# Performance work log

Hardware: AMD Instinct MI355X
Metric: run time of the kernel (lower is better)

## Reference

```python
import jax, jax.numpy as jnp
import numpy as np

CODEBOOK_SIZE = 32768
EMBED_DIM = 32
BETA = 0.25


def setup_inputs() -> dict:
    key = jax.random.key(0)
    k_z, k_cb = jax.random.split(key)
    z = jax.random.normal(k_z, (4, EMBED_DIM, 32, 32), dtype=jnp.float32)
    codebook = jax.random.normal(k_cb, (CODEBOOK_SIZE, EMBED_DIM), dtype=jnp.float32)
    return {"z": z, "codebook": codebook}


def reference(z, codebook):
    # z: [B, C, H, W] -> flatten to [N, C] tokens (channel-last, as in torch VQ)
    B, C, H, W = z.shape
    zf = jnp.transpose(z, (0, 2, 3, 1)).reshape(-1, C)  # [N, C]
    # squared L2 distance to every code: ||z||^2 - 2 z.e + ||e||^2  -> [N, K]
    d = (
        jnp.sum(zf * zf, axis=-1, keepdims=True)
        - 2.0 * (zf @ codebook.T)
        + jnp.sum(codebook * codebook, axis=-1)[None, :]
    )
    idx = jnp.argmin(d, axis=-1)  # [N]
    zq = codebook[idx].reshape(B, H, W, C).transpose(0, 3, 1, 2)  # [B, C, H, W]
    # codebook + commitment losses
    loss = jnp.mean((jax.lax.stop_gradient(zq) - z) ** 2) + BETA * jnp.mean(
        (zq - jax.lax.stop_gradient(z)) ** 2
    )
    # straight-through estimator
    zq_st = z + jax.lax.stop_gradient(zq - z)
    return zq_st, loss
```

## Files before the change

kernel.cpp:

```cpp
#include <hip/hip_runtime.h>
#include <math.h>

#define K_CB    32768
#define C_DIM   32
#define N_TOK   4096
#define OUT_N   (N_TOK * C_DIM)

#define SLICES  32
#define KPERSL  (K_CB / SLICES)
#define GROUPS  (KPERSL / 16)
#define SCALE   4096.0f

typedef _Float16 half8  __attribute__((ext_vector_type(8)));
typedef float    floatx4 __attribute__((ext_vector_type(4)));

__global__ __launch_bounds__(256) void vq_zprep(const float* __restrict__ z,
                                                _Float16* __restrict__ zh,
                                                _Float16* __restrict__ zl) {
    const int tok = blockIdx.x * 256 + threadIdx.x;
    const int b = tok >> 10, hw = tok & 1023;
    const float* zp = z + (size_t)b * (C_DIM * 1024) + hw;
    _Float16 h[C_DIM], l[C_DIM];
#pragma unroll
    for (int c = 0; c < C_DIM; ++c) {
        float xs = zp[(size_t)c * 1024] * SCALE;
        _Float16 hh = (_Float16)xs;
        h[c] = hh;
        l[c] = (_Float16)(xs - (float)hh);
    }
    half8* dh = (half8*)(zh + (size_t)tok * C_DIM);
    half8* dl = (half8*)(zl + (size_t)tok * C_DIM);
#pragma unroll
    for (int i = 0; i < 4; ++i) {
        dh[i] = *(half8*)&h[i * 8];
        dl[i] = *(half8*)&l[i * 8];
    }
}

__global__ __launch_bounds__(256) void vq_cbprep(const float* __restrict__ cb,
                                                 _Float16* __restrict__ ch,
                                                 _Float16* __restrict__ cl,
                                                 float* __restrict__ nrm,
                                                 float* __restrict__ out) {
    const int k = blockIdx.x * 256 + threadIdx.x;
    const float4* src = (const float4*)(cb + (size_t)k * C_DIM);
    _Float16 h[C_DIM], l[C_DIM];
    float s = 0.f;
#pragma unroll
    for (int i = 0; i < 8; ++i) {
        float4 v = src[i];
        s = fmaf(v.x, v.x, s); s = fmaf(v.y, v.y, s);
        s = fmaf(v.z, v.z, s); s = fmaf(v.w, v.w, s);
        float x[4] = {v.x * SCALE, v.y * SCALE, v.z * SCALE, v.w * SCALE};
#pragma unroll
        for (int j = 0; j < 4; ++j) {
            _Float16 hh = (_Float16)x[j];
            h[i * 4 + j] = hh;
            l[i * 4 + j] = (_Float16)(x[j] - (float)hh);
        }
    }
    nrm[k] = s;
    half8* dh = (half8*)(ch + (size_t)k * C_DIM);
    half8* dl = (half8*)(cl + (size_t)k * C_DIM);
#pragma unroll
    for (int i = 0; i < 4; ++i) {
        dh[i] = *(half8*)&h[i * 8];
        dl[i] = *(half8*)&l[i * 8];
    }
    if (k == 0) out[OUT_N] = 0.f;
}

__global__ __launch_bounds__(256) void vq_mfma(const _Float16* __restrict__ zh,
                                               const _Float16* __restrict__ zl,
                                               const _Float16* __restrict__ ch,
                                               const _Float16* __restrict__ cl,
                                               const float* __restrict__ nrm,
                                               float* __restrict__ pdist,
                                               int* __restrict__ pidx) {
    const int tid   = threadIdx.x;
    const int lane  = tid & 63, wid = tid >> 6;
    const int row16 = lane & 15, kgrp = lane >> 4;
    const int tile  = blockIdx.x & 31;
    const int slice = blockIdx.x >> 5;
    const int tokA  = tile * 128 + wid * 32 + row16;
    const int code0 = slice * KPERSL;

    const half8 a0h = *(const half8*)(zh + (size_t)tokA * C_DIM + kgrp * 8);
    const half8 a0l = *(const half8*)(zl + (size_t)tokA * C_DIM + kgrp * 8);
    const half8 a1h = *(const half8*)(zh + (size_t)(tokA + 16) * C_DIM + kgrp * 8);
    const half8 a1l = *(const half8*)(zl + (size_t)(tokA + 16) * C_DIM + kgrp * 8);

    const _Float16* pbh = ch + (size_t)(code0 + row16) * C_DIM + kgrp * 8;
    const _Float16* pbl = cl + (size_t)(code0 + row16) * C_DIM + kgrp * 8;
    const float*    pn  = nrm + code0 + row16;
    int kc = code0 + row16;

    float best0[4], best1[4]; int bk0[4], bk1[4];
#pragma unroll
    for (int j = 0; j < 4; ++j) {
        best0[j] = -INFINITY; best1[j] = -INFINITY; bk0[j] = 0; bk1[j] = 0;
    }

#pragma unroll 2
    for (int g = 0; g < GROUPS; ++g) {
        half8 bh = *(const half8*)pbh;
        half8 bl = *(const half8*)pbl;
        float nv = *pn;
        float initv = nv * -8388608.0f;
        floatx4 acc0 = {initv, initv, initv, initv};
        floatx4 acc1 = acc0;
        acc0 = __builtin_amdgcn_mfma_f32_16x16x32_f16(a0h, bl, acc0, 0, 0, 0);
        acc1 = __builtin_amdgcn_mfma_f32_16x16x32_f16(a1h, bl, acc1, 0, 0, 0);
        acc0 = __builtin_amdgcn_mfma_f32_16x16x32_f16(a0l, bh, acc0, 0, 0, 0);
        acc1 = __builtin_amdgcn_mfma_f32_16x16x32_f16(a1l, bh, acc1, 0, 0, 0);
        acc0 = __builtin_amdgcn_mfma_f32_16x16x32_f16(a0h, bh, acc0, 0, 0, 0);
        acc1 = __builtin_amdgcn_mfma_f32_16x16x32_f16(a1h, bh, acc1, 0, 0, 0);
#pragma unroll
        for (int j = 0; j < 4; ++j) {
            float s0 = acc0[j];
            bool g0 = s0 > best0[j];
            best0[j] = g0 ? s0 : best0[j];
            bk0[j]   = g0 ? kc : bk0[j];
            float s1 = acc1[j];
            bool g1 = s1 > best1[j];
            best1[j] = g1 ? s1 : best1[j];
            bk1[j]   = g1 ? kc : bk1[j];
        }
        pbh += 16 * C_DIM; pbl += 16 * C_DIM; pn += 16; kc += 16;
    }

#pragma unroll
    for (int off = 1; off < 16; off <<= 1) {
#pragma unroll
        for (int j = 0; j < 4; ++j) {
            float os = __shfl_xor(best0[j], off, 64);
            int   ok = __shfl_xor(bk0[j],   off, 64);
            bool t = (os > best0[j]) || (os == best0[j] && ok < bk0[j]);
            best0[j] = t ? os : best0[j];
            bk0[j]   = t ? ok : bk0[j];
            os = __shfl_xor(best1[j], off, 64);
            ok = __shfl_xor(bk1[j],   off, 64);
            t = (os > best1[j]) || (os == best1[j] && ok < bk1[j]);
            best1[j] = t ? os : best1[j];
            bk1[j]   = t ? ok : bk1[j];
        }
    }

    if (row16 == 0) {
#pragma unroll
        for (int j = 0; j < 4; ++j) {
            int r  = kgrp * 4 + j;
            int t0 = tile * 128 + wid * 32 + r;
            pdist[slice * N_TOK + t0]      = best0[j] * -1.1920928955078125e-7f;
            pidx [slice * N_TOK + t0]      = bk0[j];
            pdist[slice * N_TOK + t0 + 16] = best1[j] * -1.1920928955078125e-7f;
            pidx [slice * N_TOK + t0 + 16] = bk1[j];
        }
    }
}

__global__ __launch_bounds__(256) void vq_finalize(const float* __restrict__ z,
                                                   const float* __restrict__ cb,
                                                   const float* __restrict__ pdist,
                                                   const int* __restrict__ pidx,
                                                   float* __restrict__ out) {
    __shared__ float shd[4][64];
    __shared__ int   shk[4][64];
    __shared__ int   shbk[64];
    __shared__ float wsum[4];

    const int tok0 = blockIdx.x * 64;
    const int b = tok0 >> 10, hw0 = tok0 & 1023;
    const int tt = threadIdx.x & 63;
    const int sq = threadIdx.x >> 6;
    const int tok = tok0 + tt;

    float bd = INFINITY; int bk = 0;
    for (int s = sq * 8; s < sq * 8 + 8; ++s) {
        float d = pdist[s * N_TOK + tok];
        int   k = pidx [s * N_TOK + tok];
        if (d < bd || (d == bd && k < bk)) { bd = d; bk = k; }
    }
    shd[sq][tt] = bd; shk[sq][tt] = bk;
    __syncthreads();
    if (threadIdx.x < 64) {
        bd = shd[0][tt]; bk = shk[0][tt];
        for (int q = 1; q < 4; ++q) {
            float d = shd[q][tt]; int k = shk[q][tt];
            if (d < bd || (d == bd && k < bk)) { bd = d; bk = k; }
        }
        shbk[tt] = bk;
    }
    __syncthreads();

    const int k = shbk[tt];
    const int c0 = sq * 8;
    const float* zp = z   + (size_t)b * (C_DIM * 1024) + hw0 + tt;
    float*       op = out + (size_t)b * (C_DIM * 1024) + hw0 + tt;
    float lsum = 0.f;
#pragma unroll
    for (int c = 0; c < 8; ++c) {
        float e  = cb[(size_t)k * C_DIM + c0 + c];
        float zc = zp[(size_t)(c0 + c) * 1024];
        float df = e - zc;
        lsum = fmaf(df, df, lsum);
        op[(size_t)(c0 + c) * 1024] = e;
    }

#pragma unroll
    for (int off = 32; off > 0; off >>= 1) lsum += __shfl_down(lsum, off, 64);
    const int lane = threadIdx.x & 63, wid = threadIdx.x >> 6;
    if (lane == 0) wsum[wid] = lsum;
    __syncthreads();
    if (threadIdx.x == 0)
        atomicAdd(out + OUT_N, (wsum[0] + wsum[1] + wsum[2] + wsum[3]) * (1.25f / (float)OUT_N));
}

extern "C" void kernel_launch(void* const* d_in, const int* in_sizes, int n_in,
                              void* d_out, int out_size, void* d_ws, size_t ws_size,
                              hipStream_t stream) {
    const float* z  = (const float*)d_in[0];
    const float* cb = (const float*)d_in[1];
    float* out = (float*)d_out;

    _Float16* zh = (_Float16*)d_ws;
    _Float16* zl = zh + (size_t)N_TOK * C_DIM;
    _Float16* ch = zl + (size_t)N_TOK * C_DIM;
    _Float16* cl = ch + (size_t)K_CB * C_DIM;
    float*  norms = (float*)(cl + (size_t)K_CB * C_DIM);
    float*  pdist = norms + K_CB;
    int*    pidx  = (int*)(pdist + SLICES * N_TOK);

    vq_zprep   <<<N_TOK / 256, 256, 0, stream>>>(z, zh, zl);
    vq_cbprep  <<<K_CB / 256, 256, 0, stream>>>(cb, ch, cl, norms, out);
    vq_mfma    <<<(N_TOK / 128) * SLICES, 256, 0, stream>>>(zh, zl, ch, cl, norms, pdist, pidx);
    vq_finalize<<<N_TOK / 64, 256, 0, stream>>>(z, cb, pdist, pidx, out);
}
```

Baseline: 109.2 us.

## Merge prep kernels, enlarge token tile, and reduce argmin via 64-bit atomicMin

Combines the z and codebook prep kernels into one launch. Each wave in the MFMA kernel now covers 64 tokens instead of 32, so every codebook fragment load is reused across four MFMA groups, and the codebook is split into 64 slices. Per-slice partial results are no longer written as a distance/index array: they are packed into an order-preserving 64-bit (distance, index) key and merged with atomicMin, which lets the finalize kernel read one key per token. This removes the partial-result traffic and the reduction in finalize, at the cost of a memset launch, global atomic contention and higher register pressure.

```diff
diff --git a/kernel.cpp b/kernel.cpp
--- a/kernel.cpp
+++ b/kernel.cpp
@@ -6,68 +6,70 @@
 #define N_TOK   4096
 #define OUT_N   (N_TOK * C_DIM)
 
-#define SLICES  32
+#define SLICES  64
 #define KPERSL  (K_CB / SLICES)
 #define GROUPS  (KPERSL / 16)
 #define SCALE   4096.0f
 
-typedef _Float16 half8  __attribute__((ext_vector_type(8)));
+typedef _Float16 half8   __attribute__((ext_vector_type(8)));
 typedef float    floatx4 __attribute__((ext_vector_type(4)));
 
-__global__ __launch_bounds__(256) void vq_zprep(const float* __restrict__ z,
-                                                _Float16* __restrict__ zh,
-                                                _Float16* __restrict__ zl) {
-    const int tok = blockIdx.x * 256 + threadIdx.x;
-    const int b = tok >> 10, hw = tok & 1023;
-    const float* zp = z + (size_t)b * (C_DIM * 1024) + hw;
-    _Float16 h[C_DIM], l[C_DIM];
-#pragma unroll
-    for (int c = 0; c < C_DIM; ++c) {
-        float xs = zp[(size_t)c * 1024] * SCALE;
-        _Float16 hh = (_Float16)xs;
-        h[c] = hh;
-        l[c] = (_Float16)(xs - (float)hh);
-    }
-    half8* dh = (half8*)(zh + (size_t)tok * C_DIM);
-    half8* dl = (half8*)(zl + (size_t)tok * C_DIM);
-#pragma unroll
-    for (int i = 0; i < 4; ++i) {
-        dh[i] = *(half8*)&h[i * 8];
-        dl[i] = *(half8*)&l[i * 8];
-    }
-}
-
-__global__ __launch_bounds__(256) void vq_cbprep(const float* __restrict__ cb,
-                                                 _Float16* __restrict__ ch,
-                                                 _Float16* __restrict__ cl,
-                                                 float* __restrict__ nrm,
-                                                 float* __restrict__ out) {
-    const int k = blockIdx.x * 256 + threadIdx.x;
-    const float4* src = (const float4*)(cb + (size_t)k * C_DIM);
-    _Float16 h[C_DIM], l[C_DIM];
-    float s = 0.f;
-#pragma unroll
-    for (int i = 0; i < 8; ++i) {
-        float4 v = src[i];
-        s = fmaf(v.x, v.x, s); s = fmaf(v.y, v.y, s);
-        s = fmaf(v.z, v.z, s); s = fmaf(v.w, v.w, s);
-        float x[4] = {v.x * SCALE, v.y * SCALE, v.z * SCALE, v.w * SCALE};
-#pragma unroll
-        for (int j = 0; j < 4; ++j) {
-            _Float16 hh = (_Float16)x[j];
-            h[i * 4 + j] = hh;
-            l[i * 4 + j] = (_Float16)(x[j] - (float)hh);
-        }
-    }
-    nrm[k] = s;
-    half8* dh = (half8*)(ch + (size_t)k * C_DIM);
-    half8* dl = (half8*)(cl + (size_t)k * C_DIM);
-#pragma unroll
-    for (int i = 0; i < 4; ++i) {
-        dh[i] = *(half8*)&h[i * 8];
-        dl[i] = *(half8*)&l[i * 8];
-    }
-    if (k == 0) out[OUT_N] = 0.f;
+__global__ __launch_bounds__(256) void vq_prep(const float* __restrict__ z,
+                                               const float* __restrict__ cb,
+                                               _Float16* __restrict__ zh,
+                                               _Float16* __restrict__ zl,
+                                               _Float16* __restrict__ ch,
+                                               _Float16* __restrict__ cl,
+                                               float* __restrict__ nrm,
+                                               float* __restrict__ out) {
+    const int bb = blockIdx.x;
+    if (bb < 128) {
+        const int k = bb * 256 + threadIdx.x;
+        const float4* src = (const float4*)(cb + (size_t)k * C_DIM);
+        _Float16 h[C_DIM], l[C_DIM];
+        float s = 0.f;
+#pragma unroll
+        for (int i = 0; i < 8; ++i) {
+            float4 v = src[i];
+            s = fmaf(v.x, v.x, s); s = fmaf(v.y, v.y, s);
+            s = fmaf(v.z, v.z, s); s = fmaf(v.w, v.w, s);
+            float x[4] = {v.x * SCALE, v.y * SCALE, v.z * SCALE, v.w * SCALE};
+#pragma unroll
+            for (int j = 0; j < 4; ++j) {
+                _Float16 hh = (_Float16)x[j];
+                h[i * 4 + j] = hh;
+                l[i * 4 + j] = (_Float16)(x[j] - (float)hh);
+            }
+        }
+        nrm[k] = s;
+        half8* dh = (half8*)(ch + (size_t)k * C_DIM);
+        half8* dl = (half8*)(cl + (size_t)k * C_DIM);
+#pragma unroll
+        for (int i = 0; i < 4; ++i) {
+            dh[i] = *(half8*)&h[i * 8];
+            dl[i] = *(half8*)&l[i * 8];
+        }
+        if (k == 0) out[OUT_N] = 0.f;
+    } else {
+        const int tok = (bb - 128) * 256 + threadIdx.x;
+        const int b = tok >> 10, hw = tok & 1023;
+        const float* zp = z + (size_t)b * (C_DIM * 1024) + hw;
+        _Float16 h[C_DIM], l[C_DIM];
+#pragma unroll
+        for (int c = 0; c < C_DIM; ++c) {
+            float xs = zp[(size_t)c * 1024] * SCALE;
+            _Float16 hh = (_Float16)xs;
+            h[c] = hh;
+            l[c] = (_Float16)(xs - (float)hh);
+        }
+        half8* dh = (half8*)(zh + (size_t)tok * C_DIM);
+        half8* dl = (half8*)(zl + (size_t)tok * C_DIM);
+#pragma unroll
+        for (int i = 0; i < 4; ++i) {
+            dh[i] = *(half8*)&h[i * 8];
+            dl[i] = *(half8*)&l[i * 8];
+        }
+    }
 }
 
 __global__ __launch_bounds__(256) void vq_mfma(const _Float16* __restrict__ zh,
@@ -75,140 +77,115 @@
                                                const _Float16* __restrict__ ch,
                                                const _Float16* __restrict__ cl,
                                                const float* __restrict__ nrm,
-                                               float* __restrict__ pdist,
-                                               int* __restrict__ pidx) {
+                                               unsigned long long* __restrict__ keys) {
     const int tid   = threadIdx.x;
     const int lane  = tid & 63, wid = tid >> 6;
     const int row16 = lane & 15, kgrp = lane >> 4;
-    const int tile  = blockIdx.x & 31;
-    const int slice = blockIdx.x >> 5;
-    const int tokA  = tile * 128 + wid * 32 + row16;
+    const int tile  = blockIdx.x & 15;
+    const int slice = blockIdx.x >> 4;
+    const int tokA  = tile * 256 + wid * 64 + row16;
     const int code0 = slice * KPERSL;
 
-    const half8 a0h = *(const half8*)(zh + (size_t)tokA * C_DIM + kgrp * 8);
-    const half8 a0l = *(const half8*)(zl + (size_t)tokA * C_DIM + kgrp * 8);
-    const half8 a1h = *(const half8*)(zh + (size_t)(tokA + 16) * C_DIM + kgrp * 8);
-    const half8 a1l = *(const half8*)(zl + (size_t)(tokA + 16) * C_DIM + kgrp * 8);
+    half8 ah[4], al[4];
+#pragma unroll
+    for (int s = 0; s < 4; ++s) {
+        ah[s] = *(const half8*)(zh + (size_t)(tokA + s * 16) * C_DIM + kgrp * 8);
+        al[s] = *(const half8*)(zl + (size_t)(tokA + s * 16) * C_DIM + kgrp * 8);
+    }
 
     const _Float16* pbh = ch + (size_t)(code0 + row16) * C_DIM + kgrp * 8;
     const _Float16* pbl = cl + (size_t)(code0 + row16) * C_DIM + kgrp * 8;
     const float*    pn  = nrm + code0 + row16;
     int kc = code0 + row16;
 
-    float best0[4], best1[4]; int bk0[4], bk1[4];
-#pragma unroll
-    for (int j = 0; j < 4; ++j) {
-        best0[j] = -INFINITY; best1[j] = -INFINITY; bk0[j] = 0; bk1[j] = 0;
-    }
-
-#pragma unroll 2
+    float best[4][4]; int bk[4][4];
+#pragma unroll
+    for (int s = 0; s < 4; ++s)
+#pragma unroll
+        for (int j = 0; j < 4; ++j) { best[s][j] = -INFINITY; bk[s][j] = 0; }
+
     for (int g = 0; g < GROUPS; ++g) {
         half8 bh = *(const half8*)pbh;
         half8 bl = *(const half8*)pbl;
-        float nv = *pn;
-        float initv = nv * -8388608.0f;
-        floatx4 acc0 = {initv, initv, initv, initv};
-        floatx4 acc1 = acc0;
-        acc0 = __builtin_amdgcn_mfma_f32_16x16x32_f16(a0h, bl, acc0, 0, 0, 0);
-        acc1 = __builtin_amdgcn_mfma_f32_16x16x32_f16(a1h, bl, acc1, 0, 0, 0);
-        acc0 = __builtin_amdgcn_mfma_f32_16x16x32_f16(a0l, bh, acc0, 0, 0, 0);
-        acc1 = __builtin_amdgcn_mfma_f32_16x16x32_f16(a1l, bh, acc1, 0, 0, 0);
-        acc0 = __builtin_amdgcn_mfma_f32_16x16x32_f16(a0h, bh, acc0, 0, 0, 0);
-        acc1 = __builtin_amdgcn_mfma_f32_16x16x32_f16(a1h, bh, acc1, 0, 0, 0);
-#pragma unroll
-        for (int j = 0; j < 4; ++j) {
-            float s0 = acc0[j];
-            bool g0 = s0 > best0[j];
-            best0[j] = g0 ? s0 : best0[j];
-            bk0[j]   = g0 ? kc : bk0[j];
-            float s1 = acc1[j];
-            bool g1 = s1 > best1[j];
-            best1[j] = g1 ? s1 : best1[j];
-            bk1[j]   = g1 ? kc : bk1[j];
-        }
+        float initv = (*pn) * -8388608.0f;
+        floatx4 acc[4];
+#pragma unroll
+        for (int s = 0; s < 4; ++s) {
+            acc[s] = (floatx4){initv, initv, initv, initv};
+            acc[s] = __builtin_amdgcn_mfma_f32_16x16x32_f16(ah[s], bl, acc[s], 0, 0, 0);
+            acc[s] = __builtin_amdgcn_mfma_f32_16x16x32_f16(al[s], bh, acc[s], 0, 0, 0);
+            acc[s] = __builtin_amdgcn_mfma_f32_16x16x32_f16(ah[s], bh, acc[s], 0, 0, 0);
+        }
+#pragma unroll
+        for (int s = 0; s < 4; ++s)
+#pragma unroll
+            for (int j = 0; j < 4; ++j) {
+                float v = acc[s][j];
+                bool gt = v > best[s][j];
+                best[s][j] = gt ? v : best[s][j];
+                bk[s][j]   = gt ? kc : bk[s][j];
+            }
         pbh += 16 * C_DIM; pbl += 16 * C_DIM; pn += 16; kc += 16;
     }
 
 #pragma unroll
-    for (int off = 1; off < 16; off <<= 1) {
-#pragma unroll
-        for (int j = 0; j < 4; ++j) {
-            float os = __shfl_xor(best0[j], off, 64);
-            int   ok = __shfl_xor(bk0[j],   off, 64);
-            bool t = (os > best0[j]) || (os == best0[j] && ok < bk0[j]);
-            best0[j] = t ? os : best0[j];
-            bk0[j]   = t ? ok : bk0[j];
-            os = __shfl_xor(best1[j], off, 64);
-            ok = __shfl_xor(bk1[j],   off, 64);
-            t = (os > best1[j]) || (os == best1[j] && ok < bk1[j]);
-            best1[j] = t ? os : best1[j];
-            bk1[j]   = t ? ok : bk1[j];
-        }
-    }
+    for (int off = 1; off < 16; off <<= 1)
+#pragma unroll
+        for (int s = 0; s < 4; ++s)
+#pragma unroll
+            for (int j = 0; j < 4; ++j) {
+                float os = __shfl_xor(best[s][j], off, 64);
+                int   ok = __shfl_xor(bk[s][j],   off, 64);
+                bool t = (os > best[s][j]) || (os == best[s][j] && ok < bk[s][j]);
+                best[s][j] = t ? os : best[s][j];
+                bk[s][j]   = t ? ok : bk[s][j];
+            }
 
     if (row16 == 0) {
 #pragma unroll
-        for (int j = 0; j < 4; ++j) {
-            int r  = kgrp * 4 + j;
-            int t0 = tile * 128 + wid * 32 + r;
-            pdist[slice * N_TOK + t0]      = best0[j] * -1.1920928955078125e-7f;
-            pidx [slice * N_TOK + t0]      = bk0[j];
-            pdist[slice * N_TOK + t0 + 16] = best1[j] * -1.1920928955078125e-7f;
-            pidx [slice * N_TOK + t0 + 16] = bk1[j];
-        }
+        for (int s = 0; s < 4; ++s)
+#pragma unroll
+            for (int j = 0; j < 4; ++j) {
+                int t0 = tile * 256 + wid * 64 + s * 16 + kgrp * 4 + j;
+                float d = best[s][j] * -1.1920928955078125e-7f;
+                unsigned u = __float_as_uint(d);
+                u ^= (u & 0x80000000u) ? 0xFFFFFFFFu : 0x80000000u;
+                unsigned long long key =
+                    ((unsigned long long)u << 32) | (unsigned)bk[s][j];
+                atomicMin(keys + t0, key);
+            }
     }
 }
 
 __global__ __launch_bounds__(256) void vq_finalize(const float* __restrict__ z,
                                                    const float* __restrict__ cb,
-                                                   const float* __restrict__ pdist,
-                                                   const int* __restrict__ pidx,
+                                                   const unsigned long long* __restrict__ keys,
                                                    float* __restrict__ out) {
-    __shared__ float shd[4][64];
-    __shared__ int   shk[4][64];
-    __shared__ int   shbk[64];
-    __shared__ float wsum[4];
-
-    const int tok0 = blockIdx.x * 64;
+    const int tok0 = blockIdx.x * 32;
     const int b = tok0 >> 10, hw0 = tok0 & 1023;
-    const int tt = threadIdx.x & 63;
-    const int sq = threadIdx.x >> 6;
+    const int tt = threadIdx.x & 31;
+    const int sq = threadIdx.x >> 5;
     const int tok = tok0 + tt;
 
-    float bd = INFINITY; int bk = 0;
-    for (int s = sq * 8; s < sq * 8 + 8; ++s) {
-        float d = pdist[s * N_TOK + tok];
-        int   k = pidx [s * N_TOK + tok];
-        if (d < bd || (d == bd && k < bk)) { bd = d; bk = k; }
-    }
-    shd[sq][tt] = bd; shk[sq][tt] = bk;
-    __syncthreads();
-    if (threadIdx.x < 64) {
-        bd = shd[0][tt]; bk = shk[0][tt];
-        for (int q = 1; q < 4; ++q) {
-            float d = shd[q][tt]; int k = shk[q][tt];
-            if (d < bd || (d == bd && k < bk)) { bd = d; bk = k; }
-        }
-        shbk[tt] = bk;
-    }
-    __syncthreads();
-
-    const int k = shbk[tt];
-    const int c0 = sq * 8;
+    const int k  = (int)(keys[tok] & 0xFFFFFFFFu);
+    const int c0 = sq * 4;
+    float4 e = *(const float4*)(cb + (size_t)k * C_DIM + c0);
+    float ev[4] = {e.x, e.y, e.z, e.w};
+
     const float* zp = z   + (size_t)b * (C_DIM * 1024) + hw0 + tt;
     float*       op = out + (size_t)b * (C_DIM * 1024) + hw0 + tt;
     float lsum = 0.f;
 #pragma unroll
-    for (int c = 0; c < 8; ++c) {
-        float e  = cb[(size_t)k * C_DIM + c0 + c];
-        float zc = zp[(size_t)(c0 + c) * 1024];
-        float df = e - zc;
+    for (int j = 0; j < 4; ++j) {
+        float zc = zp[(size_t)(c0 + j) * 1024];
+        float df = ev[j] - zc;
         lsum = fmaf(df, df, lsum);
-        op[(size_t)(c0 + c) * 1024] = e;
+        op[(size_t)(c0 + j) * 1024] = ev[j];
     }
 
 #pragma unroll
     for (int off = 32; off > 0; off >>= 1) lsum += __shfl_down(lsum, off, 64);
+    __shared__ float wsum[4];
     const int lane = threadIdx.x & 63, wid = threadIdx.x >> 6;
     if (lane == 0) wsum[wid] = lsum;
     __syncthreads();
@@ -228,11 +205,10 @@
     _Float16* ch = zl + (size_t)N_TOK * C_DIM;
     _Float16* cl = ch + (size_t)K_CB * C_DIM;
     float*  norms = (float*)(cl + (size_t)K_CB * C_DIM);
-    float*  pdist = norms + K_CB;
-    int*    pidx  = (int*)(pdist + SLICES * N_TOK);
-
-    vq_zprep   <<<N_TOK / 256, 256, 0, stream>>>(z, zh, zl);
-    vq_cbprep  <<<K_CB / 256, 256, 0, stream>>>(cb, ch, cl, norms, out);
-    vq_mfma    <<<(N_TOK / 128) * SLICES, 256, 0, stream>>>(zh, zl, ch, cl, norms, pdist, pidx);
-    vq_finalize<<<N_TOK / 64, 256, 0, stream>>>(z, cb, pdist, pidx, out);
-}
+    unsigned long long* keys = (unsigned long long*)(norms + K_CB);
+
+    hipMemsetAsync(keys, 0xFF, (size_t)N_TOK * 8, stream);
+    vq_prep    <<<144, 256, 0, stream>>>(z, cb, zh, zl, ch, cl, norms, out);
+    vq_mfma    <<<(N_TOK / 256) * SLICES, 256, 0, stream>>>(zh, zl, ch, cl, norms, keys);
+    vq_finalize<<<N_TOK / 32, 256, 0, stream>>>(z, cb, keys, out);
+}
```

Measured after the change: 121.7 us. 1.11x slower.
